# Optimization experiments

Hardware: AMD Instinct MI355X
Metric: run time of the kernel (lower is better)

Reference implementation:

```python
import jax, jax.numpy as jnp
import numpy as np

THETA = 0.5  # forward default arg
ALPHA = 0.2  # LeakyReLU negative slope
NEG_INF = -9e15


def setup_inputs() -> dict:
    key = jax.random.key(0)
    k1, k2, k3, k4, k5 = jax.random.split(key, 5)
    N, F_IN, F_OUT = 8192, 256, 256
    h = jax.random.normal(k1, (N, F_IN), dtype=jnp.float32)
    adj = jax.random.randint(k2, (N, N), 0, 2, dtype=jnp.int32)
    cv_values = jax.random.uniform(k3, (N,), dtype=jnp.float32)
    # xavier_uniform with gain=1.414
    g = 1.414
    bw = g * np.sqrt(6.0 / (F_IN + F_OUT))
    W = jax.random.uniform(k4, (F_IN, F_OUT), dtype=jnp.float32, minval=-bw, maxval=bw)
    ba = g * np.sqrt(6.0 / (2 * F_OUT + 1))
    a = jax.random.uniform(k5, (2 * F_OUT, 1), dtype=jnp.float32, minval=-ba, maxval=ba)
    return {"h": h, "adj": adj, "cv_values": cv_values, "W": W, "a": a}


def reference(h, adj, cv_values, W, a):
    # Wh: [N, F_out]
    Wh = h @ W
    F_out = Wh.shape[1]
    a1 = a[:F_out, 0]   # [F_out]
    a2 = a[F_out:, 0]   # [F_out]
    # e_ij = LeakyReLU([Wh_i ; Wh_j] . a) = LeakyReLU(Wh_i.a1 + Wh_j.a2)
    f1 = Wh @ a1        # [N]
    f2 = Wh @ a2        # [N]
    e = jax.nn.leaky_relu(f1[:, None] + f2[None, :], negative_slope=ALPHA)
    # CV bias: theta * cv_i broadcast across row i
    e = e + THETA * cv_values[:, None]
    att = jnp.where(adj > 0, e, jnp.float32(NEG_INF))
    att = jax.nn.softmax(att, axis=1)
    # dropout is identity in eval mode (training=False)
    h_prime = att @ Wh  # [N, F_out]
    return jax.nn.elu(h_prime)  # concat=True branch
```

## Files before the change

kernel.cpp:

```cpp
#include <hip/hip_runtime.h>
#include <cstdint>
#include <cstddef>

typedef _Float16 half8 __attribute__((ext_vector_type(8)));
typedef _Float16 half4 __attribute__((ext_vector_type(4)));
typedef float f32x4 __attribute__((ext_vector_type(4)));

#define GAT_N 8192
#define GAT_F 256
#define GAT_NW 256
#define GAT_ALPHA 0.2f
#define GAT_LOG2E 1.4426950408889634f

__device__ inline unsigned enc_f32(float x) {
    unsigned b = __float_as_uint(x);
    return (b & 0x80000000u) ? ~b : (b | 0x80000000u);
}
__device__ inline float dec_f32(unsigned u) {
    unsigned b = (u & 0x80000000u) ? (u ^ 0x80000000u) : ~u;
    return __uint_as_float(b);
}

__global__ __launch_bounds__(256) void gat_k0_pack(
    const int* __restrict__ adj, unsigned char* __restrict__ adjB)
{
    const int wv = threadIdx.x >> 6;
    const int lane = threadIdx.x & 63;
    const int row = blockIdx.x * 4 + wv;
    const int* src = adj + (size_t)row * GAT_N;
    unsigned char* dst = adjB + (size_t)row * (GAT_N / 8);
    #pragma unroll 4
    for (int k = 0; k < 16; ++k) {
        const int4 v0 = *reinterpret_cast<const int4*>(src + k * 512 + lane * 8);
        const int4 v1 = *reinterpret_cast<const int4*>(src + k * 512 + lane * 8 + 4);
        unsigned m = (unsigned)(v0.x > 0)        | ((unsigned)(v0.y > 0) << 1)
                   | ((unsigned)(v0.z > 0) << 2) | ((unsigned)(v0.w > 0) << 3)
                   | ((unsigned)(v1.x > 0) << 4) | ((unsigned)(v1.y > 0) << 5)
                   | ((unsigned)(v1.z > 0) << 6) | ((unsigned)(v1.w > 0) << 7);
        dst[k * 64 + lane] = (unsigned char)m;
    }
}

__global__ __launch_bounds__(256) void gat_k0b_convert(
    const float* __restrict__ W, _Float16* __restrict__ WT,
    unsigned* __restrict__ f2mxEnc)
{
    const int g = blockIdx.x * 256 + threadIdx.x;
    if (g == 0) *f2mxEnc = 0u;
    const int k = g >> 8, n = g & 255;
    WT[n * GAT_F + k] = (_Float16)W[g];
}

__global__ __launch_bounds__(128) void gat_k1_gemm(
    const float* __restrict__ h, const _Float16* __restrict__ WT,
    const float* __restrict__ a, _Float16* __restrict__ whT,
    float* __restrict__ f1L, float* __restrict__ f2L,
    unsigned* __restrict__ f2mxEnc)
{
    const int wv = threadIdx.x >> 6;
    const int lane = threadIdx.x & 63;
    const int l15 = lane & 15;
    const int quad = lane >> 4;
    const int r0 = blockIdx.x * 32 + wv * 16;

    f32x4 acc[16];
    #pragma unroll
    for (int t = 0; t < 16; ++t) { f32x4 z = {0.f,0.f,0.f,0.f}; acc[t] = z; }

    #pragma unroll
    for (int k0 = 0; k0 < GAT_F; k0 += 32) {
        const float* ap = h + (size_t)(r0 + l15) * GAT_F + k0 + quad * 8;
        const float4 a0 = *reinterpret_cast<const float4*>(ap);
        const float4 a1 = *reinterpret_cast<const float4*>(ap + 4);
        half8 af;
        af[0] = (_Float16)a0.x; af[1] = (_Float16)a0.y;
        af[2] = (_Float16)a0.z; af[3] = (_Float16)a0.w;
        af[4] = (_Float16)a1.x; af[5] = (_Float16)a1.y;
        af[6] = (_Float16)a1.z; af[7] = (_Float16)a1.w;
        #pragma unroll
        for (int t = 0; t < 16; ++t) {
            half8 bf = *reinterpret_cast<const half8*>(
                WT + (size_t)(t * 16 + l15) * GAT_F + k0 + quad * 8);
            acc[t] = __builtin_amdgcn_mfma_f32_16x16x32_f16(af, bf, acc[t], 0, 0, 0);
        }
    }

    float p1[4] = {0.f,0.f,0.f,0.f}, p2[4] = {0.f,0.f,0.f,0.f};
    #pragma unroll
    for (int t = 0; t < 16; ++t) {
        float a1c = a[t * 16 + l15];
        float a2c = a[GAT_F + t * 16 + l15];
        #pragma unroll
        for (int r = 0; r < 4; ++r) {
            p1[r] = fmaf(acc[t][r], a1c, p1[r]);
            p2[r] = fmaf(acc[t][r], a2c, p2[r]);
        }
    }
    #pragma unroll
    for (int off = 1; off < 16; off <<= 1) {
        #pragma unroll
        for (int r = 0; r < 4; ++r) {
            p1[r] += __shfl_xor(p1[r], off);
            p2[r] += __shfl_xor(p2[r], off);
        }
    }
    if (l15 == 0) {
        float mx = -3.0e38f;
        #pragma unroll
        for (int r = 0; r < 4; ++r) {
            int row = r0 + quad * 4 + r;
            float s1 = p1[r] * GAT_LOG2E;
            float s2 = p2[r] * GAT_LOG2E;
            f1L[row] = s1;
            f2L[row] = s2;
            mx = fmaxf(mx, s2);
        }
        atomicMax(f2mxEnc, enc_f32(mx));
    }

    #pragma unroll
    for (int t = 0; t < 16; ++t) {
        half4 hv;
        #pragma unroll
        for (int r = 0; r < 4; ++r) hv[r] = (_Float16)acc[t][r];
        *reinterpret_cast<half4*>(
            whT + (size_t)(t * 16 + l15) * GAT_N + r0 + quad * 4) = hv;
    }
}

__global__ __launch_bounds__(256, 2) void gat_k3_attn(
    const unsigned* __restrict__ adjW, const float* __restrict__ f1L,
    const float* __restrict__ f2L, const unsigned* __restrict__ f2mxEnc,
    const _Float16* __restrict__ whT,
    _Float16* __restrict__ Ph,
    float* __restrict__ L)
{
    __shared__ __align__(16) _Float16 sB[2][256 * 32];

    const int bx = blockIdx.x;
    const int rb = bx >> 3;
    const int q  = bx & 7;
    const int wv = threadIdx.x >> 6;
    const int lane = threadIdx.x & 63;
    const int l15 = lane & 15;
    const int quad = lane >> 4;

    const int r0 = rb * 128 + wv * 32;
    const int rA = r0 + l15;
    const int rB = rA + 16;

    const float fmxL = dec_f32(*f2mxEnc);
    const float f1A = f1L[rA];
    const float f1B = f1L[rB];
    const float sA = f1A + fmxL;
    const float sBv = f1B + fmxL;
    const float CA = fmaxf(sA, GAT_ALPHA * sA);
    const float CB = fmaxf(sBv, GAT_ALPHA * sBv);

    f32x4 acc[2][16];
    #pragma unroll
    for (int s = 0; s < 2; ++s)
        #pragma unroll
        for (int t = 0; t < 16; ++t) {
            f32x4 z = {0.f,0.f,0.f,0.f};
            acc[s][t] = z;
        }
    float d0 = 0.f, d1 = 0.f;

    const int kq = q * 1024;
    const uint4* awA = reinterpret_cast<const uint4*>(adjW + (size_t)rA * GAT_NW + q * 32);
    const uint4* awB = reinterpret_cast<const uint4*>(adjW + (size_t)rB * GAT_NW + q * 32);
    const float* f2q = f2L + kq + quad * 8;

    const int sf = wv * 64 + (lane >> 2);
    const int sk = (lane & 3) * 8;
    const _Float16* gstage = whT + (size_t)sf * GAT_N + kq + sk;

    #define STAGE(buf, step)                                                   \
        {                                                                      \
            _Float16* lp = &sB[buf][(wv * 64) * 32];                           \
            const _Float16* gp = gstage + (step) * 32;                         \
            _Pragma("unroll")                                                  \
            for (int i = 0; i < 4; ++i) {                                      \
                __builtin_amdgcn_global_load_lds(                              \
                    (const __attribute__((address_space(1))) void*)            \
                        (gp + (size_t)i * 16 * GAT_N),                         \
                    (__attribute__((address_space(3))) void*)(lp + i * 512),   \
                    16, 0, 0);                                                 \
            }                                                                  \
        }

    STAGE(0, 0)
    uint4 nA = awA[0];
    uint4 nB = awB[0];
    float4 nfa = *reinterpret_cast<const float4*>(f2q);
    float4 nfb = *reinterpret_cast<const float4*>(f2q + 4);
    __syncthreads();

    for (int g = 0; g < 8; ++g) {
        const uint4 cA = nA, cB = nB;
        if (g < 7) { nA = awA[g + 1]; nB = awB[g + 1]; }

        #pragma unroll
        for (int s4 = 0; s4 < 4; ++s4) {
            const int step = g * 4 + s4;
            const int cur = step & 1;
            if (step + 1 < 32) STAGE(1 - cur, step + 1)

            const float4 cfa = nfa, cfb = nfb;
            if (step < 31) {
                nfa = *reinterpret_cast<const float4*>(f2q + (step + 1) * 32);
                nfb = *reinterpret_cast<const float4*>(f2q + (step + 1) * 32 + 4);
            }
            const unsigned wA = (s4 == 0) ? cA.x : (s4 == 1) ? cA.y : (s4 == 2) ? cA.z : cA.w;
            const unsigned wB = (s4 == 0) ? cB.x : (s4 == 1) ? cB.y : (s4 == 2) ? cB.z : cB.w;
            const unsigned mA = (wA >> (quad * 8)) & 0xffu;
            const unsigned mB = (wB >> (quad * 8)) & 0xffu;
            const float f2v[8] = {cfa.x, cfa.y, cfa.z, cfa.w, cfb.x, cfb.y, cfb.z, cfb.w};

            half8 pA, pB;
            #pragma unroll
            for (int j = 0; j < 8; ++j) {
                const float f2j = f2v[j];
                float xa = f1A + f2j;
                float la = fmaxf(xa, GAT_ALPHA * xa);
                float pa = __builtin_amdgcn_exp2f(la - CA);
                pa = (mA & (1u << j)) ? pa : 0.f;
                d0 += pa;
                pA[j] = (_Float16)pa;
                float xb = f1B + f2j;
                float lb = fmaxf(xb, GAT_ALPHA * xb);
                float pb = __builtin_amdgcn_exp2f(lb - CB);
                pb = (mB & (1u << j)) ? pb : 0.f;
                d1 += pb;
                pB[j] = (_Float16)pb;
            }

            #pragma unroll
            for (int t = 0; t < 16; ++t) {
                half8 bf = *reinterpret_cast<const half8*>(
                    &sB[cur][(t * 16 + l15) * 32 + quad * 8]);
                acc[0][t] = __builtin_amdgcn_mfma_f32_16x16x32_f16(pA, bf, acc[0][t], 0, 0, 0);
                acc[1][t] = __builtin_amdgcn_mfma_f32_16x16x32_f16(pB, bf, acc[1][t], 0, 0, 0);
            }
            __syncthreads();
        }
    }
    #undef STAGE

    d0 += __shfl_xor(d0, 16); d0 += __shfl_xor(d0, 32);
    d1 += __shfl_xor(d1, 16); d1 += __shfl_xor(d1, 32);
    float* Lq = L + q * GAT_N;
    if (lane < 16) { Lq[rA] = d0; Lq[rB] = d1; }

    const int wid = rb * 4 + wv;
    _Float16* Pq = Ph + ((size_t)q * 256 + wid) * 8192;
    #pragma unroll
    for (int s = 0; s < 2; ++s)
        #pragma unroll
        for (int t = 0; t < 16; ++t) {
            half4 hv;
            #pragma unroll
            for (int r = 0; r < 4; ++r) hv[r] = (_Float16)acc[s][t][r];
            *reinterpret_cast<half4*>(Pq + (size_t)(((s * 16 + t) * 64 + lane) * 4)) = hv;
        }
}

__global__ __launch_bounds__(256) void gat_k4_final(
    const _Float16* __restrict__ Ph, const float* __restrict__ L,
    float* __restrict__ out)
{
    const int tid = threadIdx.x;
    const int wid = blockIdx.x >> 3;
    __shared__ float s_rl[32];
    if (tid < 32) {
        const int row = wid * 32 + tid;
        float s = 0.f;
        #pragma unroll
        for (int q = 0; q < 8; ++q) s += L[q * GAT_N + row];
        s_rl[tid] = 1.0f / fmaxf(s, 1e-30f);
    }
    __syncthreads();

    const int idx = blockIdx.x * 256 + tid;
    const int rem = idx & 2047;
    const int lane = rem & 63;
    const int st = rem >> 6;
    const int s = st >> 4, t = st & 15;
    const int l15 = lane & 15, quad = lane >> 4;
    const int lrow0 = s * 16 + quad * 4;
    const int col = t * 16 + l15;

    float accv[4] = {0.f, 0.f, 0.f, 0.f};
    #pragma unroll
    for (int q = 0; q < 8; ++q) {
        half4 v = *reinterpret_cast<const half4*>(
            Ph + ((size_t)q * 256 + wid) * 8192 + (size_t)rem * 4);
        #pragma unroll
        for (int r = 0; r < 4; ++r) accv[r] += (float)v[r];
    }
    #pragma unroll
    for (int r = 0; r < 4; ++r) {
        const float v = accv[r] * s_rl[lrow0 + r];
        const float o = v > 0.f ? v : expm1f(v);
        out[(size_t)(wid * 32 + lrow0 + r) * GAT_F + col] = o;
    }
}

extern "C" void kernel_launch(void* const* d_in, const int* in_sizes, int n_in,
                              void* d_out, int out_size, void* d_ws, size_t ws_size,
                              hipStream_t stream)
{
    const float* h   = (const float*)d_in[0];
    const int*   adj = (const int*)d_in[1];
    const float* W   = (const float*)d_in[3];
    const float* a   = (const float*)d_in[4];
    float* out = (float*)d_out;
    char* ws = (char*)d_ws;

    const size_t SLAB = (size_t)GAT_N * GAT_F * 2;

    size_t off = 0;
    _Float16* whT = (_Float16*)(ws + off); off += SLAB;
    _Float16* Ph  = (_Float16*)(ws + off); off += 8 * SLAB;
    unsigned char* adjB = (unsigned char*)(ws + off); off += (size_t)GAT_N * GAT_N / 8;
    _Float16* WT  = (_Float16*)(ws + off); off += (size_t)GAT_F * GAT_F * 2;
    float* f1L = (float*)(ws + off); off += GAT_N * 4;
    float* f2L = (float*)(ws + off); off += GAT_N * 4;
    float* L   = (float*)(ws + off); off += 8 * GAT_N * 4;
    unsigned* f2mxEnc = (unsigned*)(ws + off); off += 256;

    gat_k0_pack<<<2048, 256, 0, stream>>>(adj, adjB);
    gat_k0b_convert<<<256, 256, 0, stream>>>(W, WT, f2mxEnc);
    gat_k1_gemm<<<256, 128, 0, stream>>>(h, WT, a, whT, f1L, f2L, f2mxEnc);
    gat_k3_attn<<<512, 256, 0, stream>>>((const unsigned*)adjB, f1L, f2L, f2mxEnc, whT, Ph, L);
    gat_k4_final<<<2048, 256, 0, stream>>>(Ph, L, out);
}
```

Before: 481.2 us.

## Split GEMM and attention kernels across feature halves for more blocks

The projection GEMM now gives each wave a 64-column feature slice of 16 rows, and the f1/f2 dot products are reduced across waves through shared memory. The attention kernel splits the 256 output features into two halves per block, doubling the grid and halving the accumulators and LDS staging, with launch bounds raised to 4 blocks per CU. The aim is lower register and LDS pressure, more occupancy and more parallel blocks. In exchange, the exp/softmax probability work and the adjacency loads are duplicated across the two feature halves.

Result: slower. 597.8 us (+24.2%).

```diff
diff --git a/kernel.cpp b/kernel.cpp
--- a/kernel.cpp
+++ b/kernel.cpp
@@ -51,21 +51,22 @@
     WT[n * GAT_F + k] = (_Float16)W[g];
 }
 
-__global__ __launch_bounds__(128) void gat_k1_gemm(
+__global__ __launch_bounds__(256, 2) void gat_k1_gemm(
     const float* __restrict__ h, const _Float16* __restrict__ WT,
     const float* __restrict__ a, _Float16* __restrict__ whT,
     float* __restrict__ f1L, float* __restrict__ f2L,
     unsigned* __restrict__ f2mxEnc)
 {
+    __shared__ float sP1[4][16], sP2[4][16];
     const int wv = threadIdx.x >> 6;
     const int lane = threadIdx.x & 63;
     const int l15 = lane & 15;
     const int quad = lane >> 4;
-    const int r0 = blockIdx.x * 32 + wv * 16;
-
-    f32x4 acc[16];
-    #pragma unroll
-    for (int t = 0; t < 16; ++t) { f32x4 z = {0.f,0.f,0.f,0.f}; acc[t] = z; }
+    const int r0 = blockIdx.x * 16;
+
+    f32x4 acc[4];
+    #pragma unroll
+    for (int t = 0; t < 4; ++t) { f32x4 z = {0.f,0.f,0.f,0.f}; acc[t] = z; }
 
     #pragma unroll
     for (int k0 = 0; k0 < GAT_F; k0 += 32) {
@@ -78,18 +79,18 @@
         af[4] = (_Float16)a1.x; af[5] = (_Float16)a1.y;
         af[6] = (_Float16)a1.z; af[7] = (_Float16)a1.w;
         #pragma unroll
-        for (int t = 0; t < 16; ++t) {
+        for (int t = 0; t < 4; ++t) {
             half8 bf = *reinterpret_cast<const half8*>(
-                WT + (size_t)(t * 16 + l15) * GAT_F + k0 + quad * 8);
+                WT + (size_t)(wv * 64 + t * 16 + l15) * GAT_F + k0 + quad * 8);
             acc[t] = __builtin_amdgcn_mfma_f32_16x16x32_f16(af, bf, acc[t], 0, 0, 0);
         }
     }
 
     float p1[4] = {0.f,0.f,0.f,0.f}, p2[4] = {0.f,0.f,0.f,0.f};
     #pragma unroll
-    for (int t = 0; t < 16; ++t) {
-        float a1c = a[t * 16 + l15];
-        float a2c = a[GAT_F + t * 16 + l15];
+    for (int t = 0; t < 4; ++t) {
+        float a1c = a[wv * 64 + t * 16 + l15];
+        float a2c = a[GAT_F + wv * 64 + t * 16 + l15];
         #pragma unroll
         for (int r = 0; r < 4; ++r) {
             p1[r] = fmaf(acc[t][r], a1c, p1[r]);
@@ -105,41 +106,48 @@
         }
     }
     if (l15 == 0) {
-        float mx = -3.0e38f;
         #pragma unroll
         for (int r = 0; r < 4; ++r) {
-            int row = r0 + quad * 4 + r;
-            float s1 = p1[r] * GAT_LOG2E;
-            float s2 = p2[r] * GAT_LOG2E;
-            f1L[row] = s1;
-            f2L[row] = s2;
-            mx = fmaxf(mx, s2);
-        }
-        atomicMax(f2mxEnc, enc_f32(mx));
-    }
-
-    #pragma unroll
-    for (int t = 0; t < 16; ++t) {
+            sP1[wv][quad * 4 + r] = p1[r];
+            sP2[wv][quad * 4 + r] = p2[r];
+        }
+    }
+    __syncthreads();
+    if (threadIdx.x < 16) {
+        const int row = threadIdx.x;
+        const float s1 = (sP1[0][row] + sP1[1][row] + sP1[2][row] + sP1[3][row]) * GAT_LOG2E;
+        const float s2 = (sP2[0][row] + sP2[1][row] + sP2[2][row] + sP2[3][row]) * GAT_LOG2E;
+        f1L[r0 + row] = s1;
+        f2L[r0 + row] = s2;
+        float mx = s2;
+        #pragma unroll
+        for (int off = 1; off < 16; off <<= 1) mx = fmaxf(mx, __shfl_xor(mx, off));
+        if (row == 0) atomicMax(f2mxEnc, enc_f32(mx));
+    }
+
+    #pragma unroll
+    for (int t = 0; t < 4; ++t) {
         half4 hv;
         #pragma unroll
         for (int r = 0; r < 4; ++r) hv[r] = (_Float16)acc[t][r];
         *reinterpret_cast<half4*>(
-            whT + (size_t)(t * 16 + l15) * GAT_N + r0 + quad * 4) = hv;
-    }
-}
-
-__global__ __launch_bounds__(256, 2) void gat_k3_attn(
+            whT + (size_t)(wv * 64 + t * 16 + l15) * GAT_N + r0 + quad * 4) = hv;
+    }
+}
+
+__global__ __launch_bounds__(256, 4) void gat_k3_attn(
     const unsigned* __restrict__ adjW, const float* __restrict__ f1L,
     const float* __restrict__ f2L, const unsigned* __restrict__ f2mxEnc,
     const _Float16* __restrict__ whT,
     _Float16* __restrict__ Ph,
     float* __restrict__ L)
 {
-    __shared__ __align__(16) _Float16 sB[2][256 * 32];
+    __shared__ __align__(16) _Float16 sB[2][128 * 32];
 
     const int bx = blockIdx.x;
-    const int rb = bx >> 3;
     const int q  = bx & 7;
+    const int fh = (bx >> 3) & 1;
+    const int rb = bx >> 4;
     const int wv = threadIdx.x >> 6;
     const int lane = threadIdx.x & 63;
     const int l15 = lane & 15;
@@ -157,11 +165,11 @@
     const float CA = fmaxf(sA, GAT_ALPHA * sA);
     const float CB = fmaxf(sBv, GAT_ALPHA * sBv);
 
-    f32x4 acc[2][16];
+    f32x4 acc[2][8];
     #pragma unroll
     for (int s = 0; s < 2; ++s)
         #pragma unroll
-        for (int t = 0; t < 16; ++t) {
+        for (int t = 0; t < 8; ++t) {
             f32x4 z = {0.f,0.f,0.f,0.f};
             acc[s][t] = z;
         }
@@ -172,22 +180,21 @@
     const uint4* awB = reinterpret_cast<const uint4*>(adjW + (size_t)rB * GAT_NW + q * 32);
     const float* f2q = f2L + kq + quad * 8;
 
-    const int sf = wv * 64 + (lane >> 2);
-    const int sk = (lane & 3) * 8;
-    const _Float16* gstage = whT + (size_t)sf * GAT_N + kq + sk;
+    const _Float16* gstage = whT
+        + (size_t)(fh * 128 + wv * 32 + (lane >> 2)) * GAT_N + kq + (lane & 3) * 8;
 
     #define STAGE(buf, step)                                                   \
         {                                                                      \
-            _Float16* lp = &sB[buf][(wv * 64) * 32];                           \
+            _Float16* lp = &sB[buf][wv * 1024];                                \
             const _Float16* gp = gstage + (step) * 32;                         \
-            _Pragma("unroll")                                                  \
-            for (int i = 0; i < 4; ++i) {                                      \
-                __builtin_amdgcn_global_load_lds(                              \
-                    (const __attribute__((address_space(1))) void*)            \
-                        (gp + (size_t)i * 16 * GAT_N),                         \
-                    (__attribute__((address_space(3))) void*)(lp + i * 512),   \
-                    16, 0, 0);                                                 \
-            }                                                                  \
+            __builtin_amdgcn_global_load_lds(                                  \
+                (const __attribute__((address_space(1))) void*)gp,             \
+                (__attribute__((address_space(3))) void*)lp, 16, 0, 0);        \
+            __builtin_amdgcn_global_load_lds(                                  \
+                (const __attribute__((address_space(1))) void*)                \
+                    (gp + (size_t)16 * GAT_N),                                 \
+                (__attribute__((address_space(3))) void*)(lp + 512),           \
+                16, 0, 0);                                                     \
         }
 
     STAGE(0, 0)
@@ -237,7 +244,7 @@
             }
 
             #pragma unroll
-            for (int t = 0; t < 16; ++t) {
+            for (int t = 0; t < 8; ++t) {
                 half8 bf = *reinterpret_cast<const half8*>(
                     &sB[cur][(t * 16 + l15) * 32 + quad * 8]);
                 acc[0][t] = __builtin_amdgcn_mfma_f32_16x16x32_f16(pA, bf, acc[0][t], 0, 0, 0);
@@ -250,19 +257,22 @@
 
     d0 += __shfl_xor(d0, 16); d0 += __shfl_xor(d0, 32);
     d1 += __shfl_xor(d1, 16); d1 += __shfl_xor(d1, 32);
-    float* Lq = L + q * GAT_N;
-    if (lane < 16) { Lq[rA] = d0; Lq[rB] = d1; }
+    if (fh == 0 && lane < 16) {
+        float* Lq = L + q * GAT_N;
+        Lq[rA] = d0; Lq[rB] = d1;
+    }
 
     const int wid = rb * 4 + wv;
     _Float16* Pq = Ph + ((size_t)q * 256 + wid) * 8192;
     #pragma unroll
     for (int s = 0; s < 2; ++s)
         #pragma unroll
-        for (int t = 0; t < 16; ++t) {
+        for (int t = 0; t < 8; ++t) {
+            const int tt = fh * 8 + t;
             half4 hv;
             #pragma unroll
             for (int r = 0; r < 4; ++r) hv[r] = (_Float16)acc[s][t][r];
-            *reinterpret_cast<half4*>(Pq + (size_t)(((s * 16 + t) * 64 + lane) * 4)) = hv;
+            *reinterpret_cast<half4*>(Pq + (size_t)(((s * 16 + tt) * 64 + lane) * 4)) = hv;
         }
 }
 
@@ -332,7 +342,7 @@
 
     gat_k0_pack<<<2048, 256, 0, stream>>>(adj, adjB);
     gat_k0b_convert<<<256, 256, 0, stream>>>(W, WT, f2mxEnc);
-    gat_k1_gemm<<<256, 128, 0, stream>>>(h, WT, a, whT, f1L, f2L, f2mxEnc);
-    gat_k3_attn<<<512, 256, 0, stream>>>((const unsigned*)adjB, f1L, f2L, f2mxEnc, whT, Ph, L);
+    gat_k1_gemm<<<512, 256, 0, stream>>>(h, WT, a, whT, f1L, f2L, f2mxEnc);
+    gat_k3_attn<<<1024, 256, 0, stream>>>((const unsigned*)adjB, f1L, f2L, f2mxEnc, whT, Ph, L);
     gat_k4_final<<<2048, 256, 0, stream>>>(Ph, L, out);
 }
```
